# Kernel tuning notes

Hardware: AMD Instinct MI355X
Metric: run time of the kernel (lower is better)

## Reference

```python
import jax, jax.numpy as jnp
import numpy as np

B, T, D = 2, 2048, 2048
N_HEADS, N_KV, HEAD_DIM = 16, 8, 128
SOFTCAP = 50.0
BIG_NEG = -2.3819763e38
ROPE_BASE = 10000.0


def apply_rope(x, positions):
    # x: [B, L, N, H], positions: [B, L]
    H = x.shape[-1]
    half = H // 2
    fraction = 2.0 * jnp.arange(half, dtype=jnp.float32) / H
    timescale = ROPE_BASE ** fraction  # [H/2]
    sinusoid = positions.astype(jnp.float32)[:, :, None, None] / timescale[None, None, None, :]  # [B,L,1,H/2]
    sin, cos = jnp.sin(sinusoid), jnp.cos(sinusoid)
    first, second = jnp.split(x, 2, axis=-1)
    out = jnp.concatenate([first * cos - second * sin, second * cos + first * sin], axis=-1)
    return out.astype(x.dtype)


def setup_inputs() -> dict:
    key = jax.random.key(0)
    k1, k2, k3, k4 = jax.random.split(key, 4)
    x = jax.random.normal(k1, (B, T, D), dtype=jnp.float32)
    positions = jnp.broadcast_to(jnp.arange(T, dtype=jnp.int32), (B, T))
    # causal mask [B, 1, T, S]
    attn_mask = jnp.broadcast_to(jnp.tril(jnp.ones((T, T), dtype=bool))[None, None], (B, 1, T, T))
    s = 1.0 / np.sqrt(D)
    w_q = jax.random.normal(k2, (N_HEADS, D, HEAD_DIM), dtype=jnp.float32) * s
    w_kv = jax.random.normal(k3, (2, N_KV, D, HEAD_DIM), dtype=jnp.float32) * s
    w_out = jax.random.normal(k4, (N_HEADS, HEAD_DIM, D), dtype=jnp.float32) * (1.0 / np.sqrt(N_HEADS * HEAD_DIM))
    return {"x": x, "positions": positions, "attn_mask": attn_mask, "w_q": w_q, "w_kv": w_kv, "w_out": w_out}


def reference(x, positions, attn_mask, w_q, w_kv, w_out):
    # projections (GQA branch: num_kv_heads != num_heads)
    q = jnp.einsum('btd,ndh->btnh', x, w_q)            # [B,T,N,H]
    kv = jnp.einsum('bsd,cndh->cbsnh', x, w_kv)        # [2,B,S,K,H]
    k, v = kv[0], kv[1]
    q = apply_rope(q, positions) * (HEAD_DIM ** -0.5)  # rsqrt_head_dim
    k = apply_rope(k, positions)
    G = N_HEADS // N_KV
    q = q.reshape(B, T, N_KV, G, HEAD_DIM)             # B T K G H
    logits = jnp.einsum('btkgh,bskh->bkgts', q, k).astype(jnp.float32)
    logits = jnp.tanh(logits / SOFTCAP) * SOFTCAP
    masked = jnp.where(attn_mask[:, :, None, :, :], logits, BIG_NEG)
    probs = jax.nn.softmax(masked, axis=-1).astype(k.dtype)
    encoded = jnp.einsum('bkgts,bskh->btkgh', probs, v).reshape(B, T, N_HEADS, HEAD_DIM)
    return jnp.einsum('btnh,nhd->btd', encoded, w_out)
```

## Files before the change

kernel.cpp:

```cpp
#include <hip/hip_runtime.h>


typedef unsigned short u16;
typedef __attribute__((ext_vector_type(8))) short short8;
typedef __attribute__((ext_vector_type(4))) float floatx4;

static __device__ __forceinline__ u16 f2b(float f){
  unsigned u = __float_as_uint(f);
  u = (u + 0x7fffu + ((u >> 16) & 1u)) >> 16;
  return (u16)u;
}
static __device__ __forceinline__ float b2f(u16 u){
  return __uint_as_float(((unsigned)u) << 16);
}
static __device__ __forceinline__ void gload16(const u16* g, u16* l){
  __builtin_amdgcn_global_load_lds(
      (const __attribute__((address_space(1))) unsigned int*)g,
      (__attribute__((address_space(3))) unsigned int*)l, 16, 0, 0);
}

static __device__ void tr64(const float* __restrict__ s, u16* __restrict__ d,
                            int sRS, int dRS, float (*t)[65], int tid){
  #pragma unroll
  for(int i = 0; i < 16; i++){
    int idx = tid + 256 * i;
    t[idx >> 6][idx & 63] = s[(long)(idx >> 6) * sRS + (idx & 63)];
  }
  __syncthreads();
  #pragma unroll
  for(int i = 0; i < 16; i++){
    int idx = tid + 256 * i;
    d[(long)(idx >> 6) * dRS + (idx & 63)] = f2b(t[idx & 63][idx >> 6]);
  }
}

__global__ __launch_bounds__(256) void k_prep(
    const float* __restrict__ x, u16* __restrict__ xb,
    const float* __restrict__ wq, u16* __restrict__ wq_t,
    const float* __restrict__ wkv, u16* __restrict__ wkv_t,
    const float* __restrict__ wo, u16* __restrict__ wo_t,
    const int* __restrict__ pos, float* __restrict__ tab){
  __shared__ float t[64][65];
  int blk = blockIdx.x, tid = threadIdx.x;
  if(blk < 8192){
    int i = blk * 256 + tid;
    float4 v = ((const float4*)x)[i];
    ushort4 o = make_ushort4(f2b(v.x), f2b(v.y), f2b(v.z), f2b(v.w));
    ((ushort4*)xb)[i] = o;
  } else if(blk < 9216){
    int q = blk - 8192;
    int bx = q & 1, by = (q >> 1) & 31, bz = q >> 6;
    tr64(wq + (long)bz * 262144 + (long)by * 64 * 128 + bx * 64,
         wq_t + (long)bz * 262144 + (long)bx * 64 * 2048 + by * 64, 128, 2048, t, tid);
  } else if(blk < 10240){
    int q = blk - 9216;
    int bx = q & 1, by = (q >> 1) & 31, bz = q >> 6;
    tr64(wkv + (long)bz * 262144 + (long)by * 64 * 128 + bx * 64,
         wkv_t + (long)bz * 262144 + (long)bx * 64 * 2048 + by * 64, 128, 2048, t, tid);
  } else if(blk < 11264){
    int q = blk - 10240;
    int bx = q & 31, by = q >> 5;
    tr64(wo + (long)by * 64 * 2048 + bx * 64,
         wo_t + (long)bx * 64 * 2048 + by * 64, 2048, 2048, t, tid);
  } else {
    int idx = (blk - 11264) * 256 + tid;
    int row = idx >> 6, h = idx & 63;
    float pf = (float)pos[row];
    float inv = exp2f(-0.20762050593045077f * (float)h);
    float ang = pf * inv;
    tab[(row << 7) + h]      = sinf(ang);
    tab[(row << 7) + 64 + h] = cosf(ang);
  }
}

#define QKV_BAR() do{ __builtin_amdgcn_s_barrier(); \
                      __builtin_amdgcn_sched_barrier(0); }while(0)
#define STAGE_A(tt, h) do{ \
  const u16* s_ = Ag + (tt) * 64 + (h) * 262144; \
  u16* d_ = ld + ss * 8192; \
  gload16(s_, d_); gload16(s_ + 131072, d_ + 4096); \
  ss++; if(ss == 10) ss = 0; }while(0)
#define STAGE_B(tt, h) do{ \
  const u16* s_ = Bg + (tt) * 64 + (h) * 262144; \
  u16* d_ = ld + ss * 8192; \
  gload16(s_, d_); gload16(s_ + 131072, d_ + 4096); \
  ss++; if(ss == 10) ss = 0; }while(0)

__global__ __launch_bounds__(512, 2) void k_gemm_qkv(
    const u16* __restrict__ A, const u16* __restrict__ wq_t, const u16* __restrict__ wkv_t,
    const float* __restrict__ tab,
    u16* __restrict__ qb, u16* __restrict__ kb, u16* __restrict__ vtp){
  __shared__ __attribute__((aligned(16))) u16 ring[81920];
  int mt = blockIdx.x, nt = blockIdx.y;
  const u16* Bt = (nt < 8) ? (wq_t + (long)nt * 524288)
                           : (wkv_t + (long)(nt - 8) * 524288);
  int tid = threadIdx.x;
  int lane = tid & 63, wave = tid >> 6, l15 = lane & 15, quad = lane >> 4;
  int wr = wave >> 2, wc = wave & 3;
  int cq0 = quad ^ (l15 & 7), cq1 = cq0 ^ 4;
  int srow = tid >> 3;
  int gch  = (tid & 7) ^ (srow & 7);
  const u16* Ag = A  + ((long)mt * 256 + srow) * 2048 + (gch << 3);
  const u16* Bg = Bt + (long)srow * 2048 + (gch << 3);
  u16* ld = ring + tid * 8;
  int aB = l15 << 6;
  int bB = ((wc & 1) * 64 + l15) << 6;
  int sa = wr;
  int sb = 2 + (wc >> 1);
  int ss = 0;
  floatx4 acc[8][4];
  const floatx4 fz = {0.f, 0.f, 0.f, 0.f};
  #pragma unroll
  for(int m = 0; m < 8; m++)
    #pragma unroll
    for(int n = 0; n < 4; n++) acc[m][n] = fz;

  STAGE_A(0, 0); STAGE_A(0, 1); STAGE_B(0, 0); STAGE_B(0, 1);
  STAGE_A(1, 0); STAGE_A(1, 1);
  asm volatile("s_waitcnt vmcnt(4)" ::: "memory");
  QKV_BAR();

  #pragma unroll 1
  for(int t = 0; t < 32; t++){
    const u16* aS = ring + sa * 8192;
    const u16* bS = ring + sb * 8192;
    int tB = (t < 31) ? t + 1 : 31;
    int tA = (t < 30) ? t + 2 : 31;
    short8 af[4], bfr[4];
    #pragma unroll
    for(int n = 0; n < 4; n++) bfr[n] = *(const short8*)(bS + bB + (n << 10) + (cq0 << 3));
    #pragma unroll
    for(int m = 0; m < 4; m++) af[m]  = *(const short8*)(aS + aB + (m << 10) + (cq0 << 3));
    STAGE_B(tB, 0);
    QKV_BAR();
    __builtin_amdgcn_s_setprio(1);
    #pragma unroll
    for(int m = 0; m < 4; m++)
      #pragma unroll
      for(int n = 0; n < 4; n++)
        acc[m][n] = __builtin_amdgcn_mfma_f32_16x16x32_bf16(af[m], bfr[n], acc[m][n], 0, 0, 0);
    __builtin_amdgcn_s_setprio(0);
    QKV_BAR();
    #pragma unroll
    for(int m = 0; m < 4; m++) af[m] = *(const short8*)(aS + aB + 4096 + (m << 10) + (cq0 << 3));
    STAGE_B(tB, 1);
    QKV_BAR();
    __builtin_amdgcn_s_setprio(1);
    #pragma unroll
    for(int m = 0; m < 4; m++)
      #pragma unroll
      for(int n = 0; n < 4; n++)
        acc[4 + m][n] = __builtin_amdgcn_mfma_f32_16x16x32_bf16(af[m], bfr[n], acc[4 + m][n], 0, 0, 0);
    __builtin_amdgcn_s_setprio(0);
    QKV_BAR();
    #pragma unroll
    for(int n = 0; n < 4; n++) bfr[n] = *(const short8*)(bS + bB + (n << 10) + (cq1 << 3));
    #pragma unroll
    for(int m = 0; m < 4; m++) af[m]  = *(const short8*)(aS + aB + (m << 10) + (cq1 << 3));
    STAGE_A(tA, 0);
    QKV_BAR();
    __builtin_amdgcn_s_setprio(1);
    #pragma unroll
    for(int m = 0; m < 4; m++)
      #pragma unroll
      for(int n = 0; n < 4; n++)
        acc[m][n] = __builtin_amdgcn_mfma_f32_16x16x32_bf16(af[m], bfr[n], acc[m][n], 0, 0, 0);
    __builtin_amdgcn_s_setprio(0);
    QKV_BAR();
    #pragma unroll
    for(int m = 0; m < 4; m++) af[m] = *(const short8*)(aS + aB + 4096 + (m << 10) + (cq1 << 3));
    STAGE_A(tA, 1);
    asm volatile("s_waitcnt vmcnt(4)" ::: "memory");
    __builtin_amdgcn_sched_barrier(0);
    QKV_BAR();
    __builtin_amdgcn_s_setprio(1);
    #pragma unroll
    for(int m = 0; m < 4; m++)
      #pragma unroll
      for(int n = 0; n < 4; n++)
        acc[4 + m][n] = __builtin_amdgcn_mfma_f32_16x16x32_bf16(af[m], bfr[n], acc[4 + m][n], 0, 0, 0);
    __builtin_amdgcn_s_setprio(0);
    QKV_BAR();
    sa += 4; if(sa >= 10) sa -= 10;
    sb += 4; if(sb >= 10) sb -= 10;
  }

  asm volatile("s_waitcnt vmcnt(0)" ::: "memory");
  __syncthreads();
  u16* sT = ring;
  int grow0 = mt * 256;
  int hb = wc >> 1, wcl = wc & 1;
  #pragma unroll 1
  for(int hh = 0; hh < 2; hh++){
    if(hb == hh){
      #pragma unroll
      for(int m = 0; m < 8; m++){
        int row = wr * 128 + m * 16 + quad * 4;
        #pragma unroll
        for(int n = 0; n < 4; n++){
          int colh = wcl * 64 + n * 16 + l15;
          #pragma unroll
          for(int j = 0; j < 4; j++)
            sT[(row + j) * 132 + colh] = f2b(acc[m][n][j]);
        }
      }
    }
    __syncthreads();
    if(nt < 12){
      float scale = (nt < 8) ? 0.08838834764831845f : 1.0f;
      u16* dst = (nt < 8) ? qb : kb;
      int dS   = (nt < 8) ? 2048 : 1024;
      int dcol = (nt < 8) ? (nt * 2 + hh) * 128 : ((nt - 8) * 2 + hh) * 128;
      #pragma unroll
      for(int it = 0; it < 16; it++){
        int idx = tid + 512 * it;
        int row = idx >> 5, cw = idx & 31;
        int grow = grow0 + row;
        unsigned lo = *(const unsigned*)&sT[row * 132 + 2 * cw];
        unsigned hi = *(const unsigned*)&sT[row * 132 + 64 + 2 * cw];
        float2 sn = *(const float2*)&tab[(grow << 7) + 2 * cw];
        float2 cs = *(const float2*)&tab[(grow << 7) + 64 + 2 * cw];
        float x1a = b2f((u16)lo), x1b = b2f((u16)(lo >> 16));
        float x2a = b2f((u16)hi), x2b = b2f((u16)(hi >> 16));
        float o1a = (x1a * cs.x - x2a * sn.x) * scale;
        float o1b = (x1b * cs.y - x2b * sn.y) * scale;
        float o2a = (x2a * cs.x + x1a * sn.x) * scale;
        float o2b = (x2b * cs.y + x1b * sn.y) * scale;
        unsigned w1 = (unsigned)f2b(o1a) | ((unsigned)f2b(o1b) << 16);
        unsigned w2 = (unsigned)f2b(o2a) | ((unsigned)f2b(o2b) << 16);
        *(unsigned*)&dst[(long)grow * dS + dcol + 2 * cw] = w1;
        *(unsigned*)&dst[(long)grow * dS + dcol + 64 + 2 * cw] = w2;
      }
    } else {
      int b = mt >> 3, kvh = (nt - 12) * 2 + hh;
      u16* vt = vtp + (long)(b * 8 + kvh) * 262144;
      int tcol0 = (mt & 7) * 256;
      int h = tid >> 2, s0 = (tid & 3) * 64;
      #pragma unroll
      for(int i = 0; i < 16; i++){
        int s = s0 + i * 4;
        ushort4 v4 = make_ushort4(sT[(s    ) * 132 + h], sT[(s + 1) * 132 + h],
                                  sT[(s + 2) * 132 + h], sT[(s + 3) * 132 + h]);
        *(ushort4*)&vt[(long)h * 2048 + tcol0 + s] = v4;
      }
    }
    __syncthreads();
  }
}
#undef STAGE_A
#undef STAGE_B
#undef QKV_BAR

__global__ __launch_bounds__(256) void k_gemm_out(
    const u16* __restrict__ A, const u16* __restrict__ Bt0, float* __restrict__ C){
  __shared__ __attribute__((aligned(16))) u16 sA[128 * 64];
  __shared__ __attribute__((aligned(16))) u16 sB[128 * 64];
  int mt = blockIdx.x, nt = blockIdx.y;
  const u16* Bt = Bt0 + (long)nt * 262144;
  int tid = threadIdx.x;
  int lane = tid & 63, wave = tid >> 6, l15 = lane & 15, quad = lane >> 4;
  int ro = (wave & 1) * 64, co = (wave >> 1) * 64;
  int xm7 = l15 & 7;
  int srow = tid >> 3;
  int gch  = (tid & 7) ^ (srow & 7);
  const u16* Ag = A  + ((long)(mt * 128) + srow) * 2048 + (gch << 3);
  const u16* Bg = Bt + (long)srow * 2048 + (gch << 3);
  u16* lA = sA + tid * 8;
  u16* lB = sB + tid * 8;
  floatx4 acc[4][4];
  const floatx4 fz = {0.f, 0.f, 0.f, 0.f};
  #pragma unroll
  for(int r = 0; r < 4; r++)
    #pragma unroll
    for(int c = 0; c < 4; c++) acc[r][c] = fz;
  for(int k0 = 0; k0 < 2048; k0 += 64){
    #pragma unroll
    for(int r = 0; r < 4; r++){
      gload16(Ag + (long)r * 65536 + k0, lA + r * 2048);
      gload16(Bg + (long)r * 65536 + k0, lB + r * 2048);
    }
    __syncthreads();
    #pragma unroll
    for(int ks = 0; ks < 2; ks++){
      short8 af[4], bfr[4];
      #pragma unroll
      for(int r = 0; r < 4; r++)
        af[r]  = *(const short8*)(sA + ((ro + r * 16 + l15) << 6) + ((((ks << 2) | quad) ^ xm7) << 3));
      #pragma unroll
      for(int c = 0; c < 4; c++)
        bfr[c] = *(const short8*)(sB + ((co + c * 16 + l15) << 6) + ((((ks << 2) | quad) ^ xm7) << 3));
      #pragma unroll
      for(int r = 0; r < 4; r++)
        #pragma unroll
        for(int c = 0; c < 4; c++)
          acc[r][c] = __builtin_amdgcn_mfma_f32_16x16x32_bf16(af[r], bfr[c], acc[r][c], 0, 0, 0);
    }
    __syncthreads();
  }
  long rb0 = (long)mt * 128 + ro + quad * 4;
  #pragma unroll
  for(int r = 0; r < 4; r++)
    #pragma unroll
    for(int c = 0; c < 4; c++){
      int col = nt * 128 + co + c * 16 + l15;
      #pragma unroll
      for(int j = 0; j < 4; j++)
        C[(rb0 + r * 16 + j) * 2048 + col] = acc[r][c][j];
    }
}

__global__ __launch_bounds__(256) void k_flash(
    const u16* __restrict__ qb, const u16* __restrict__ kb,
    const u16* __restrict__ vt, u16* __restrict__ enc){
  __shared__ __attribute__((aligned(16))) u16 sK[2 * 64 * 128];
  __shared__ __attribute__((aligned(16))) u16 sVt[2 * 128 * 64];
  __shared__ __attribute__((aligned(16))) u16 sP[4][16][72];
  int qt = 31 - blockIdx.y;
  int hidx = blockIdx.x;
  int b = hidx >> 4, kv = (hidx >> 1) & 7, g = hidx & 1;
  int tid = threadIdx.x;
  int lane = tid & 63, wave = tid >> 6, l15 = lane & 15, quad = lane >> 4;

  short8 qf[4];
  {
    const u16* qg = qb + ((long)b * 2048 + qt * 64 + wave * 16 + l15) * 2048
                       + (kv * 2 + g) * 128 + quad * 8;
    #pragma unroll
    for(int ks = 0; ks < 4; ks++) qf[ks] = *(const short8*)(qg + ks * 32);
  }

  int krow = tid >> 4;
  int kch  = (tid & 15) ^ krow;
  const u16* Kg = kb + ((long)b * 2048 + krow) * 1024 + kv * 128 + (kch << 3);
  int vrow = tid >> 3;
  int vch  = (tid & 7) ^ (vrow & 7);
  const u16* Vg = vt + ((long)(b * 8 + kv) * 128 + vrow) * 2048 + (vch << 3);
  u16* lK = sK  + tid * 8;
  u16* lV = sVt + tid * 8;
  #pragma unroll
  for(int r = 0; r < 4; r++){
    gload16(Kg + (long)r * 16384, lK + r * 2048);
    gload16(Vg + (long)r * 65536, lV + r * 2048);
  }

  float l_loc[4] = {0.f, 0.f, 0.f, 0.f};
  floatx4 o_acc[8];
  const floatx4 fz = {0.f, 0.f, 0.f, 0.f};
  #pragma unroll
  for(int c = 0; c < 8; c++) o_acc[c] = fz;

  const float c1 = 0.057707801635558536f;
  const float c2 = -144.26950408889634f;
  const float c3 = 72.13475204444817f;

  for(int kt = 0; kt <= qt; kt++){
    int buf = (kt & 1) * 8192;
    __syncthreads();
    if(kt < qt){
      int nb = buf ^ 8192;
      #pragma unroll
      for(int r = 0; r < 4; r++){
        gload16(Kg + (long)(kt + 1) * 65536 + (long)r * 16384, lK + nb + r * 2048);
        gload16(Vg + (kt + 1) * 64 + (long)r * 65536, lV + nb + r * 2048);
      }
    }
    floatx4 s_acc[4];
    #pragma unroll
    for(int c = 0; c < 4; c++) s_acc[c] = fz;
    #pragma unroll
    for(int ks = 0; ks < 4; ks++){
      #pragma unroll
      for(int cb = 0; cb < 4; cb++){
        short8 bk = *(const short8*)(sK + buf + ((cb * 16 + l15) << 7)
                                     + ((((ks << 2) | quad) ^ l15) << 3));
        s_acc[cb] = __builtin_amdgcn_mfma_f32_16x16x32_bf16(qf[ks], bk, s_acc[cb], 0, 0, 0);
      }
    }
    if(kt < qt){
      #pragma unroll
      for(int r = 0; r < 4; r++){
        #pragma unroll
        for(int cb = 0; cb < 4; cb++){
          float s = s_acc[cb][r];
          float u = __builtin_amdgcn_exp2f(c1 * s);
          float d = __builtin_amdgcn_rcpf(u + 1.f);
          float p = __builtin_amdgcn_exp2f(__builtin_fmaf(c2, d, c3));
          l_loc[r] += p;
          sP[wave][quad * 4 + r][cb * 16 + l15] = f2b(p);
        }
      }
    } else {
      int rloc = wave * 16 + quad * 4;
      #pragma unroll
      for(int r = 0; r < 4; r++){
        #pragma unroll
        for(int cb = 0; cb < 4; cb++){
          float s = s_acc[cb][r];
          float u = __builtin_amdgcn_exp2f(c1 * s);
          float d = __builtin_amdgcn_rcpf(u + 1.f);
          float p = __builtin_amdgcn_exp2f(__builtin_fmaf(c2, d, c3));
          if(cb * 16 + l15 > rloc + r) p = 0.f;
          l_loc[r] += p;
          sP[wave][quad * 4 + r][cb * 16 + l15] = f2b(p);
        }
      }
    }
    #pragma unroll
    for(int ks2 = 0; ks2 < 2; ks2++){
      short8 ap = *(const short8*)&sP[wave][l15][ks2 * 32 + quad * 8];
      #pragma unroll
      for(int c = 0; c < 8; c++){
        short8 bv = *(const short8*)(sVt + buf + ((c * 16 + l15) << 6)
                                     + ((((ks2 << 2) | quad) ^ (l15 & 7)) << 3));
        o_acc[c] = __builtin_amdgcn_mfma_f32_16x16x32_bf16(ap, bv, o_acc[c], 0, 0, 0);
      }
    }
  }
  #pragma unroll
  for(int r = 0; r < 4; r++){
    float l = l_loc[r];
    #pragma unroll
    for(int off = 1; off < 16; off <<= 1) l += __shfl_xor(l, off);
    float invl = 1.f / l;
    long rowe = (long)b * 2048 + qt * 64 + wave * 16 + quad * 4 + r;
    #pragma unroll
    for(int c = 0; c < 8; c++)
      enc[rowe * 2048 + (kv * 2 + g) * 128 + c * 16 + l15] = f2b(o_acc[c][r] * invl);
  }
}

extern "C" void kernel_launch(void* const* d_in, const int* in_sizes, int n_in,
                              void* d_out, int out_size, void* d_ws, size_t ws_size,
                              hipStream_t stream){
  const float* x     = (const float*)d_in[0];
  const int*   posi  = (const int*)  d_in[1];
  const float* w_q   = (const float*)d_in[3];
  const float* w_kv  = (const float*)d_in[4];
  const float* w_out = (const float*)d_in[5];
  float* out = (float*)d_out;

  char* w = (char*)d_ws;
  u16* xb     = (u16*)(w);
  u16* wq_t   = (u16*)(w + 16777216);
  u16* wkv_t  = (u16*)(w + 25165824);
  u16* wout_t = (u16*)(w + 33554432);
  u16* q_buf  = (u16*)(w + 41943040);
  u16* k_buf  = (u16*)(w + 58720256);
  u16* v_t    = (u16*)(w + 67108864);
  float* tab  = (float*)(w + 75497472);
  u16* enc    = xb;

  k_prep    <<<12288, 256, 0, stream>>>(x, xb, w_q, wq_t, w_kv, wkv_t, w_out, wout_t, posi, tab);
  k_gemm_qkv<<<dim3(16, 16), 512, 0, stream>>>(xb, wq_t, wkv_t, tab, q_buf, k_buf, v_t);
  k_flash   <<<dim3(32, 32), 256, 0, stream>>>(q_buf, k_buf, v_t, enc);
  k_gemm_out<<<dim3(32, 16), 256, 0, stream>>>(enc, wout_t, out);
}
```

Baseline: 325.9 us.

## Reorder QKV GEMM inner loop into N-split quadrants and drop sched barriers

The QKV projection GEMM main loop now walks the 8x4 accumulator grid in quadrants, splitting N into two halves instead of splitting K. Each phase loads both K-halves of its fragments and issues two chained MFMA passes. The compiler sched_barriers are removed, and explicit lgkmcnt waits after each s_barrier take over the LDS-read ordering. The aim is to cut how many B fragments are live at once, cut redundant LDS reloads, and give the scheduler more freedom. The cost is back-to-back dependent MFMAs on the same accumulators, and removing the sched_barriers may let the compiler reorder across phases in unexpected ways.

Result: no change. 323.0 us (-0.9%).

```diff
diff --git a/kernel.cpp b/kernel.cpp
--- a/kernel.cpp
+++ b/kernel.cpp
@@ -73,8 +73,6 @@
   }
 }
 
-#define QKV_BAR() do{ __builtin_amdgcn_s_barrier(); \
-                      __builtin_amdgcn_sched_barrier(0); }while(0)
 #define STAGE_A(tt, h) do{ \
   const u16* s_ = Ag + (tt) * 64 + (h) * 262144; \
   u16* d_ = ld + ss * 8192; \
@@ -118,7 +116,7 @@
   STAGE_A(0, 0); STAGE_A(0, 1); STAGE_B(0, 0); STAGE_B(0, 1);
   STAGE_A(1, 0); STAGE_A(1, 1);
   asm volatile("s_waitcnt vmcnt(4)" ::: "memory");
-  QKV_BAR();
+  __builtin_amdgcn_s_barrier();
 
   #pragma unroll 1
   for(int t = 0; t < 32; t++){
@@ -126,61 +124,97 @@
     const u16* bS = ring + sb * 8192;
     int tB = (t < 31) ? t + 1 : 31;
     int tA = (t < 30) ? t + 2 : 31;
-    short8 af[4], bfr[4];
-    #pragma unroll
-    for(int n = 0; n < 4; n++) bfr[n] = *(const short8*)(bS + bB + (n << 10) + (cq0 << 3));
-    #pragma unroll
-    for(int m = 0; m < 4; m++) af[m]  = *(const short8*)(aS + aB + (m << 10) + (cq0 << 3));
+    short8 a0[4], a1[4], b0[2], b1[2];
+    #pragma unroll
+    for(int n = 0; n < 2; n++){
+      b0[n] = *(const short8*)(bS + bB + (n << 10) + (cq0 << 3));
+      b1[n] = *(const short8*)(bS + bB + (n << 10) + (cq1 << 3));
+    }
+    #pragma unroll
+    for(int m = 0; m < 4; m++){
+      a0[m] = *(const short8*)(aS + aB + (m << 10) + (cq0 << 3));
+      a1[m] = *(const short8*)(aS + aB + (m << 10) + (cq1 << 3));
+    }
     STAGE_B(tB, 0);
-    QKV_BAR();
+    __builtin_amdgcn_s_barrier();
+    asm volatile("s_waitcnt lgkmcnt(0)");
     __builtin_amdgcn_s_setprio(1);
     #pragma unroll
     for(int m = 0; m < 4; m++)
       #pragma unroll
-      for(int n = 0; n < 4; n++)
-        acc[m][n] = __builtin_amdgcn_mfma_f32_16x16x32_bf16(af[m], bfr[n], acc[m][n], 0, 0, 0);
+      for(int n = 0; n < 2; n++)
+        acc[m][n] = __builtin_amdgcn_mfma_f32_16x16x32_bf16(a0[m], b0[n], acc[m][n], 0, 0, 0);
+    #pragma unroll
+    for(int m = 0; m < 4; m++)
+      #pragma unroll
+      for(int n = 0; n < 2; n++)
+        acc[m][n] = __builtin_amdgcn_mfma_f32_16x16x32_bf16(a1[m], b1[n], acc[m][n], 0, 0, 0);
     __builtin_amdgcn_s_setprio(0);
-    QKV_BAR();
-    #pragma unroll
-    for(int m = 0; m < 4; m++) af[m] = *(const short8*)(aS + aB + 4096 + (m << 10) + (cq0 << 3));
+    __builtin_amdgcn_s_barrier();
+    #pragma unroll
+    for(int m = 0; m < 4; m++){
+      a0[m] = *(const short8*)(aS + aB + 4096 + (m << 10) + (cq0 << 3));
+      a1[m] = *(const short8*)(aS + aB + 4096 + (m << 10) + (cq1 << 3));
+    }
     STAGE_B(tB, 1);
-    QKV_BAR();
+    __builtin_amdgcn_s_barrier();
+    asm volatile("s_waitcnt lgkmcnt(0)");
     __builtin_amdgcn_s_setprio(1);
     #pragma unroll
     for(int m = 0; m < 4; m++)
       #pragma unroll
-      for(int n = 0; n < 4; n++)
-        acc[4 + m][n] = __builtin_amdgcn_mfma_f32_16x16x32_bf16(af[m], bfr[n], acc[4 + m][n], 0, 0, 0);
+      for(int n = 0; n < 2; n++)
+        acc[4 + m][n] = __builtin_amdgcn_mfma_f32_16x16x32_bf16(a0[m], b0[n], acc[4 + m][n], 0, 0, 0);
+    #pragma unroll
+    for(int m = 0; m < 4; m++)
+      #pragma unroll
+      for(int n = 0; n < 2; n++)
+        acc[4 + m][n] = __builtin_amdgcn_mfma_f32_16x16x32_bf16(a1[m], b1[n], acc[4 + m][n], 0, 0, 0);
     __builtin_amdgcn_s_setprio(0);
-    QKV_BAR();
-    #pragma unroll
-    for(int n = 0; n < 4; n++) bfr[n] = *(const short8*)(bS + bB + (n << 10) + (cq1 << 3));
-    #pragma unroll
-    for(int m = 0; m < 4; m++) af[m]  = *(const short8*)(aS + aB + (m << 10) + (cq1 << 3));
+    __builtin_amdgcn_s_barrier();
+    #pragma unroll
+    for(int n = 0; n < 2; n++){
+      b0[n] = *(const short8*)(bS + bB + ((2 + n) << 10) + (cq0 << 3));
+      b1[n] = *(const short8*)(bS + bB + ((2 + n) << 10) + (cq1 << 3));
+    }
     STAGE_A(tA, 0);
-    QKV_BAR();
+    __builtin_amdgcn_s_barrier();
+    asm volatile("s_waitcnt lgkmcnt(0)");
     __builtin_amdgcn_s_setprio(1);
     #pragma unroll
     for(int m = 0; m < 4; m++)
       #pragma unroll
-      for(int n = 0; n < 4; n++)
-        acc[m][n] = __builtin_amdgcn_mfma_f32_16x16x32_bf16(af[m], bfr[n], acc[m][n], 0, 0, 0);
+      for(int n = 0; n < 2; n++)
+        acc[4 + m][2 + n] = __builtin_amdgcn_mfma_f32_16x16x32_bf16(a0[m], b0[n], acc[4 + m][2 + n], 0, 0, 0);
+    #pragma unroll
+    for(int m = 0; m < 4; m++)
+      #pragma unroll
+      for(int n = 0; n < 2; n++)
+        acc[4 + m][2 + n] = __builtin_amdgcn_mfma_f32_16x16x32_bf16(a1[m], b1[n], acc[4 + m][2 + n], 0, 0, 0);
     __builtin_amdgcn_s_setprio(0);
-    QKV_BAR();
-    #pragma unroll
-    for(int m = 0; m < 4; m++) af[m] = *(const short8*)(aS + aB + 4096 + (m << 10) + (cq1 << 3));
+    __builtin_amdgcn_s_barrier();
+    #pragma unroll
+    for(int m = 0; m < 4; m++){
+      a0[m] = *(const short8*)(aS + aB + (m << 10) + (cq0 << 3));
+      a1[m] = *(const short8*)(aS + aB + (m << 10) + (cq1 << 3));
+    }
     STAGE_A(tA, 1);
     asm volatile("s_waitcnt vmcnt(4)" ::: "memory");
-    __builtin_amdgcn_sched_barrier(0);
-    QKV_BAR();
+    __builtin_amdgcn_s_barrier();
+    asm volatile("s_waitcnt lgkmcnt(0)");
     __builtin_amdgcn_s_setprio(1);
     #pragma unroll
     for(int m = 0; m < 4; m++)
       #pragma unroll
-      for(int n = 0; n < 4; n++)
-        acc[4 + m][n] = __builtin_amdgcn_mfma_f32_16x16x32_bf16(af[m], bfr[n], acc[4 + m][n], 0, 0, 0);
+      for(int n = 0; n < 2; n++)
+        acc[m][2 + n] = __builtin_amdgcn_mfma_f32_16x16x32_bf16(a0[m], b0[n], acc[m][2 + n], 0, 0, 0);
+    #pragma unroll
+    for(int m = 0; m < 4; m++)
+      #pragma unroll
+      for(int n = 0; n < 2; n++)
+        acc[m][2 + n] = __builtin_amdgcn_mfma_f32_16x16x32_bf16(a1[m], b1[n], acc[m][2 + n], 0, 0, 0);
     __builtin_amdgcn_s_setprio(0);
-    QKV_BAR();
+    __builtin_amdgcn_s_barrier();
     sa += 4; if(sa >= 10) sa -= 10;
     sb += 4; if(sb >= 10) sb -= 10;
   }
@@ -249,7 +283,6 @@
 }
 #undef STAGE_A
 #undef STAGE_B
-#undef QKV_BAR
 
 __global__ __launch_bounds__(256) void k_gemm_out(
     const u16* __restrict__ A, const u16* __restrict__ Bt0, float* __restrict__ C){
```
